# Performance work log

Measured on AMD Instinct MI355X. Metric: run time of the kernel, lower is better.

## Reference

```python
import jax, jax.numpy as jnp
import numpy as np

DIM = 2048
LAT = 512          # dim / compression_factor
NH = 16
NKV = 4
HD = LAT // NH     # 32
KVD = NKV * HD     # 128
K = 3              # conv kernel
GAIN = 0.25
EPS = 1e-6
THETA = 10000.0


def _rms(x, g):
    x32 = x.astype(jnp.float32)
    r = jax.lax.rsqrt(jnp.mean(x32 * x32, axis=-1, keepdims=True) + EPS)
    return (x32 * r).astype(x.dtype) * g.astype(x.dtype)


def _causal_conv(x, w, groups):
    # x: [B,S,C], w: [C, C//groups, K]; left-pad K-1 == pad both + trim right
    xc = jnp.transpose(x, (0, 2, 1))
    y = jax.lax.conv_general_dilated(
        xc, w, window_strides=(1,), padding=[(K - 1, 0)],
        feature_group_count=groups, dimension_numbers=('NCH', 'OIH', 'NCH'))
    return jnp.transpose(y, (0, 2, 1))


def _rope_tables(S):
    freqs = 1.0 / THETA ** (jnp.arange(0, HD, 2, dtype=jnp.float32) / HD)
    t = jnp.arange(S, dtype=jnp.float32)
    f = jnp.outer(t, freqs)               # [S, HD/2]
    return jnp.cos(f), jnp.sin(f)


def _rope(x, cos, sin):
    # x: [B,H,S,HD]; interleaved even/odd rotation
    x1, x2 = x[..., ::2], x[..., 1::2]
    r1 = x1 * cos - x2 * sin
    r2 = x1 * sin + x2 * cos
    return jnp.stack([r1, r2], axis=-1).reshape(x.shape)


def setup_inputs() -> dict:
    key = jax.random.key(0)
    ks = jax.random.split(key, 8)
    s = 0.02
    return {
        'x': jax.random.normal(ks[0], (4, 2048, DIM), jnp.float32),
        'w_q': jax.random.normal(ks[1], (LAT, DIM), jnp.float32) * s,
        'w_k': jax.random.normal(ks[2], (KVD, DIM), jnp.float32) * s,
        'w_v': jax.random.normal(ks[3], (KVD, DIM), jnp.float32) * s,
        'g_latent': jnp.ones((LAT,), jnp.float32),
        'g_kv': jnp.ones((KVD,), jnp.float32),
        'conv_q_w': jax.random.normal(ks[4], (LAT, LAT // NH, K), jnp.float32) * s,
        'conv_k_w': jax.random.normal(ks[5], (KVD, KVD // NKV, K), jnp.float32) * s,
        'g_conv': jnp.ones((LAT,), jnp.float32),
        'g_kconv': jnp.ones((KVD,), jnp.float32),
        'g_postq': jnp.ones((LAT,), jnp.float32),
        'g_postk': jnp.ones((KVD,), jnp.float32),
        'key_temp': jnp.ones((1,), jnp.float32),
        'g_preout': jnp.ones((LAT,), jnp.float32),
        'w_o': jax.random.normal(ks[6], (DIM, LAT), jnp.float32) * s,
    }


def reference(x, w_q, w_k, w_v, g_latent, g_kv, conv_q_w, conv_k_w,
              g_conv, g_kconv, g_postq, g_postk, key_temp, g_preout, w_o):
    B, S, D = x.shape
    n_groups = NH // NKV

    q = _rms(x @ w_q.T, g_latent)          # [B,S,LAT]
    k = _rms(x @ w_k.T, g_kv)              # [B,S,KVD]
    v = _rms(x @ w_v.T, g_kv)
    q_pre, k_pre = q, k

    q = _rms(_causal_conv(q, conv_q_w, NH), g_conv)
    k = _rms(_causal_conv(k, conv_k_w, NKV), g_kconv)

    # qk-mean modulation (n_groups > 1 branch)
    q_mean = q_pre.reshape(B, S, NH, HD).mean(axis=2)    # [B,S,HD]
    k_mean = k_pre.reshape(B, S, NKV, HD).mean(axis=2)   # [B,S,HD]
    q = q + GAIN * jnp.broadcast_to(k_mean[:, :, None, :], (B, S, NH, HD)).reshape(B, S, LAT)
    k = k + GAIN * jnp.broadcast_to(q_mean[:, :, None, :], (B, S, NKV, HD)).reshape(B, S, KVD)

    q = _rms(q, g_postq)
    k = _rms(k, g_postk)

    q = q.reshape(B, S, NH, HD).transpose(0, 2, 1, 3)    # [B,NH,S,HD]
    k = k.reshape(B, S, NKV, HD).transpose(0, 2, 1, 3)   # [B,NKV,S,HD]
    v = v.reshape(B, S, NKV, HD).transpose(0, 2, 1, 3)

    # QK L2 norm with learnable key temperature
    sqrt_hd = jnp.sqrt(jnp.float32(HD))
    qn = jnp.maximum(jnp.linalg.norm(q, axis=-1, keepdims=True), 1e-12)
    kn = jnp.maximum(jnp.linalg.norm(k, axis=-1, keepdims=True), 1e-12)
    q = q / qn * sqrt_hd
    k = k / kn * sqrt_hd * key_temp[0]

    cos, sin = _rope_tables(S)
    q = _rope(q, cos, sin)
    k = _rope(k, cos, sin)

    # GQA expand kv heads
    k = jnp.broadcast_to(k[:, :, None], (B, NKV, n_groups, S, HD)).reshape(B, NH, S, HD)
    v = jnp.broadcast_to(v[:, :, None], (B, NKV, n_groups, S, HD)).reshape(B, NH, S, HD)

    scale = HD ** -0.5
    scores = jnp.einsum('bhqd,bhkd->bhqk', q, k) * scale
    causal = jnp.tril(jnp.ones((S, S), bool))
    scores = jnp.where(causal, scores, jnp.finfo(scores.dtype).min)
    attn = jax.nn.softmax(scores, axis=-1)
    out = jnp.einsum('bhqk,bhkd->bhqd', attn, v)

    out = out.transpose(0, 2, 1, 3).reshape(B, S, LAT)
    out = _rms(out, g_preout)
    return out @ w_o.T
```

## Files before the change

kernel.cpp:

```cpp
#include <hip/hip_runtime.h>
#include <hip/hip_bf16.h>
#include <math.h>

constexpr int S_LEN = 2048;
constexpr int B_SZ  = 4;
constexpr int NROWS = B_SZ * S_LEN;
constexpr float GAIN_  = 0.25f;
constexpr float EPS_   = 1e-6f;
constexpr float THETA_ = 10000.0f;
constexpr float LOG2E_ = 1.44269504f;

typedef __attribute__((ext_vector_type(8))) short short8;
typedef __attribute__((ext_vector_type(4))) short sshort4;
typedef __attribute__((ext_vector_type(4))) float float4v;

__device__ __forceinline__ short f2bs(float f) {
    __hip_bfloat16 h = __float2bfloat16(f);
    short r;
    __builtin_memcpy(&r, &h, 2);
    return r;
}

__device__ __forceinline__ void async_copy16(const short* g, short* l) {
    __builtin_amdgcn_global_load_lds(
        (const __attribute__((address_space(1))) void*)g,
        (__attribute__((address_space(3))) void*)l, 16, 0, 0);
}

__device__ __forceinline__ int xcd_remap(int nwg) {
    int orig = blockIdx.x + gridDim.x * (blockIdx.y + gridDim.y * blockIdx.z);
    return (orig & 7) * (nwg >> 3) + (orig >> 3);
}

__device__ __forceinline__ float block_reduce_sum_256(float v, float* scratch) {
    __syncthreads();
    for (int off = 32; off > 0; off >>= 1)
        v += __shfl_down(v, off, 64);
    int lane = threadIdx.x & 63;
    int wid  = threadIdx.x >> 6;
    if (lane == 0) scratch[wid] = v;
    __syncthreads();
    return scratch[0] + scratch[1] + scratch[2] + scratch[3];
}

__device__ __forceinline__ void block_reduce_sum2_256(float& a, float& b, float* scratch) {
    __syncthreads();
    for (int off = 32; off > 0; off >>= 1) {
        a += __shfl_down(a, off, 64);
        b += __shfl_down(b, off, 64);
    }
    int lane = threadIdx.x & 63;
    int wid  = threadIdx.x >> 6;
    if (lane == 0) { scratch[wid] = a; scratch[4 + wid] = b; }
    __syncthreads();
    a = scratch[0] + scratch[1] + scratch[2] + scratch[3];
    b = scratch[4] + scratch[5] + scratch[6] + scratch[7];
}

__device__ __forceinline__ void block_reduce_sum3_256(float& a, float& b, float& c, float* scratch) {
    __syncthreads();
    for (int off = 32; off > 0; off >>= 1) {
        a += __shfl_down(a, off, 64);
        b += __shfl_down(b, off, 64);
        c += __shfl_down(c, off, 64);
    }
    int lane = threadIdx.x & 63;
    int wid  = threadIdx.x >> 6;
    if (lane == 0) { scratch[wid] = a; scratch[4 + wid] = b; scratch[8 + wid] = c; }
    __syncthreads();
    a = scratch[0] + scratch[1] + scratch[2] + scratch[3];
    b = scratch[4] + scratch[5] + scratch[6] + scratch[7];
    c = scratch[8] + scratch[9] + scratch[10] + scratch[11];
}

__global__ __launch_bounds__(256) void cvt_bf16(
    const float* __restrict__ src, short* __restrict__ dst, int n) {
    int i = (blockIdx.x * 256 + threadIdx.x) * 4;
    if (i >= n) return;
    float4 v = *(const float4*)(src + i);
    sshort4 o;
    o.x = f2bs(v.x); o.y = f2bs(v.y); o.z = f2bs(v.z); o.w = f2bs(v.w);
    *(sshort4*)(dst + i) = o;
}

__global__ __launch_bounds__(256) void cvt_weights(
    const float* __restrict__ wq, const float* __restrict__ wk,
    const float* __restrict__ wv, const float* __restrict__ wo,
    short* __restrict__ wqkvb, short* __restrict__ wob) {
    int i = (blockIdx.x * 256 + threadIdx.x) * 4;
    const float* src;
    short* dst;
    int j;
    if (i < 1048576)      { src = wq; dst = wqkvb + i; j = i; }
    else if (i < 1310720) { src = wk; dst = wqkvb + i; j = i - 1048576; }
    else if (i < 1572864) { src = wv; dst = wqkvb + i; j = i - 1310720; }
    else                  { src = wo; dst = wob + (i - 1572864); j = i - 1572864; }
    float4 v = *(const float4*)(src + j);
    sshort4 o;
    o.x = f2bs(v.x); o.y = f2bs(v.y); o.z = f2bs(v.z); o.w = f2bs(v.w);
    *(sshort4*)dst = o;
}

__global__ __launch_bounds__(256) void gemm_bf16_mfma(
    const short* __restrict__ A, const short* __restrict__ B,
    float* __restrict__ C, int N, int K) {
    __shared__ short As[128 * 32];
    __shared__ short Bs[128 * 32];
    int tid = threadIdx.x;
    int wave = tid >> 6, lane = tid & 63;
    int wg = xcd_remap(gridDim.x * gridDim.y);
    int bx = wg % gridDim.x, by = wg / gridDim.x;
    int m0 = by * 128, n0 = bx * 128;
    int wm = (wave >> 1) * 64, wn = (wave & 1) * 64;
    int mrow = lane & 15, quad = lane >> 4;
    float4v acc[4][4] = {};
    for (int k0 = 0; k0 < K; k0 += 32) {
        __syncthreads();
#pragma unroll
        for (int p = 0; p < 2; ++p) {
            int f = p * 256 + tid;
            int row = f >> 2, ch = (f & 3) * 8;
            const short* ga = A + (size_t)(m0 + row) * K + k0 + ch;
            const short* gb = B + (size_t)(n0 + row) * K + k0 + ch;
            async_copy16(ga, As + p * 2048 + wave * 512);
            async_copy16(gb, Bs + p * 2048 + wave * 512);
        }
        __syncthreads();
        short8 af[4], bf[4];
#pragma unroll
        for (int i = 0; i < 4; ++i)
            af[i] = *(const short8*)&As[(wm + i * 16 + mrow) * 32 + quad * 8];
#pragma unroll
        for (int j = 0; j < 4; ++j)
            bf[j] = *(const short8*)&Bs[(wn + j * 16 + mrow) * 32 + quad * 8];
#pragma unroll
        for (int i = 0; i < 4; ++i)
#pragma unroll
            for (int j = 0; j < 4; ++j)
                acc[i][j] = __builtin_amdgcn_mfma_f32_16x16x32_bf16(af[i], bf[j], acc[i][j], 0, 0, 0);
    }
#pragma unroll
    for (int i = 0; i < 4; ++i)
#pragma unroll
        for (int r = 0; r < 4; ++r) {
            int m = m0 + wm + i * 16 + quad * 4 + r;
            float* crow = C + (size_t)m * N + n0 + wn;
#pragma unroll
            for (int j = 0; j < 4; ++j)
                crow[j * 16 + mrow] = acc[i][j][r];
        }
}

__global__ __launch_bounds__(256) void gemm_bf16_mfma_sk2(
    const short* __restrict__ A, const short* __restrict__ B,
    float* __restrict__ C0, float* __restrict__ C1, int N, int K) {
    __shared__ short As[128 * 32];
    __shared__ short Bs[128 * 32];
    int tid = threadIdx.x;
    int wave = tid >> 6, lane = tid & 63;
    int wg = xcd_remap(gridDim.x * gridDim.y * gridDim.z);
    int bx = wg % gridDim.x;
    int t  = wg / gridDim.x;
    int by = t % gridDim.y;
    int bz = t / gridDim.y;
    int m0 = by * 128, n0 = bx * 128;
    int wm = (wave >> 1) * 64, wn = (wave & 1) * 64;
    int mrow = lane & 15, quad = lane >> 4;
    int kh = K >> 1;
    int kbeg = bz * kh, kend = kbeg + kh;
    float* __restrict__ C = bz ? C1 : C0;
    float4v acc[4][4] = {};
    for (int k0 = kbeg; k0 < kend; k0 += 32) {
        __syncthreads();
#pragma unroll
        for (int p = 0; p < 2; ++p) {
            int f = p * 256 + tid;
            int row = f >> 2, ch = (f & 3) * 8;
            const short* ga = A + (size_t)(m0 + row) * K + k0 + ch;
            const short* gb = B + (size_t)(n0 + row) * K + k0 + ch;
            async_copy16(ga, As + p * 2048 + wave * 512);
            async_copy16(gb, Bs + p * 2048 + wave * 512);
        }
        __syncthreads();
        short8 af[4], bf[4];
#pragma unroll
        for (int i = 0; i < 4; ++i)
            af[i] = *(const short8*)&As[(wm + i * 16 + mrow) * 32 + quad * 8];
#pragma unroll
        for (int j = 0; j < 4; ++j)
            bf[j] = *(const short8*)&Bs[(wn + j * 16 + mrow) * 32 + quad * 8];
#pragma unroll
        for (int i = 0; i < 4; ++i)
#pragma unroll
            for (int j = 0; j < 4; ++j)
                acc[i][j] = __builtin_amdgcn_mfma_f32_16x16x32_bf16(af[i], bf[j], acc[i][j], 0, 0, 0);
    }
#pragma unroll
    for (int i = 0; i < 4; ++i)
#pragma unroll
        for (int r = 0; r < 4; ++r) {
            int m = m0 + wm + i * 16 + quad * 4 + r;
            float* crow = C + (size_t)m * N + n0 + wn;
#pragma unroll
            for (int j = 0; j < 4; ++j)
                crow[j * 16 + mrow] = acc[i][j][r];
        }
}

__global__ __launch_bounds__(256) void rms_qkv_means(
    float* __restrict__ qkv, const float* __restrict__ qkv2,
    const float* __restrict__ g_latent, const float* __restrict__ g_kv,
    float* __restrict__ qmean, float* __restrict__ kmean,
    short* __restrict__ vtb) {
    int row = blockIdx.x;
    int b = row >> 11, s = row & (S_LEN - 1);
    float* p = qkv + (size_t)row * 768;
    const float* p2 = qkv2 + (size_t)row * 768;
    __shared__ float sh[640];
    __shared__ float scratch[12];
    int tid = threadIdx.x;
    float v0 = p[tid] + p2[tid];
    float v1 = p[tid + 256] + p2[tid + 256];
    float v2 = p[tid + 512] + p2[tid + 512];
    float sq = v0 * v0 + v1 * v1;
    float sk = (tid < 128) ? v2 * v2 : 0.f;
    float sv = (tid >= 128) ? v2 * v2 : 0.f;
    block_reduce_sum3_256(sq, sk, sv, scratch);
    float rq = rsqrtf(sq / 512.f + EPS_);
    float q0 = v0 * rq * g_latent[tid];
    float q1 = v1 * rq * g_latent[tid + 256];
    p[tid] = q0; p[tid + 256] = q1;
    sh[tid] = q0; sh[tid + 256] = q1;
    if (tid < 128) {
        float rk = rsqrtf(sk / 128.f + EPS_);
        float kv = v2 * rk * g_kv[tid];
        p[512 + tid] = kv; sh[512 + tid] = kv;
    } else {
        float rv = rsqrtf(sv / 128.f + EPS_);
        float vv = v2 * rv * g_kv[tid - 128];
        int d_full = tid - 128;
        vtb[((size_t)(b * 4 + (d_full >> 5)) * 32 + (d_full & 31)) * S_LEN + s] = f2bs(vv);
    }
    __syncthreads();
    if (tid < 32) {
        float sm = 0.f;
#pragma unroll
        for (int h = 0; h < 16; ++h) sm += sh[h * 32 + tid];
        qmean[(size_t)row * 32 + tid] = sm * (1.f / 16.f);
    } else if (tid < 64) {
        int d = tid - 32;
        float sm = 0.f;
#pragma unroll
        for (int h = 0; h < 4; ++h) sm += sh[512 + h * 32 + d];
        kmean[(size_t)row * 32 + d] = sm * 0.25f;
    }
}

__global__ __launch_bounds__(256) void causal_conv32(
    const float* __restrict__ in, int ldin, int inoff,
    const float* __restrict__ w, float* __restrict__ out, int C) {
    int b = blockIdx.z, g = blockIdx.y, s0 = blockIdx.x * 32;
    __shared__ float wsh[32][3][32];
    __shared__ float ish[34][33];
    int tid = threadIdx.x;
    for (int i = tid; i < 32 * 96; i += 256) {
        int oc = i / 96, r = i % 96;
        wsh[r / 3][r % 3][oc] = w[(size_t)(g * 32 + oc) * 96 + r];
    }
    for (int i = tid; i < 34 * 32; i += 256) {
        int pp = i >> 5, ic = i & 31;
        int s = s0 - 2 + pp;
        ish[pp][ic] = (s >= 0) ? in[((size_t)b * S_LEN + s) * ldin + inoff + g * 32 + ic] : 0.f;
    }
    __syncthreads();
    int sl = tid >> 3, oc0 = (tid & 7) * 4;
    float acc[4] = {0.f, 0.f, 0.f, 0.f};
    for (int ic = 0; ic < 32; ++ic) {
        float x0 = ish[sl][ic], x1 = ish[sl + 1][ic], x2 = ish[sl + 2][ic];
#pragma unroll
        for (int j = 0; j < 4; ++j)
            acc[j] += x0 * wsh[ic][0][oc0 + j] + x1 * wsh[ic][1][oc0 + j] + x2 * wsh[ic][2][oc0 + j];
    }
    float* orow = out + ((size_t)b * S_LEN + s0 + sl) * C + g * 32 + oc0;
    orow[0] = acc[0]; orow[1] = acc[1]; orow[2] = acc[2]; orow[3] = acc[3];
}

__global__ __launch_bounds__(256) void mix_rows(
    const float* __restrict__ convq, const float* __restrict__ convk,
    const float* __restrict__ qmean, const float* __restrict__ kmean,
    const float* __restrict__ g_conv, const float* __restrict__ g_kconv,
    const float* __restrict__ g_postq, const float* __restrict__ g_postk,
    const float* __restrict__ key_temp,
    short* __restrict__ qb, short* __restrict__ kb) {
    int row = blockIdx.x;
    int s = row & (S_LEN - 1);
    int tid = threadIdx.x;
    __shared__ float sh[640];
    __shared__ float scratch[8];
    __shared__ float hscale[20];
    float q0 = convq[(size_t)row * 512 + tid];
    float q1 = convq[(size_t)row * 512 + tid + 256];
    float k0 = (tid < 128) ? convk[(size_t)row * 128 + tid] : 0.f;
    float ssq = q0 * q0 + q1 * q1;
    float ssk = k0 * k0;
    block_reduce_sum2_256(ssq, ssk, scratch);
    float r1  = rsqrtf(ssq / 512.f + EPS_);
    float rk1 = rsqrtf(ssk / 128.f + EPS_);
    float km = kmean[(size_t)row * 32 + (tid & 31)];
    float a0 = q0 * r1 * g_conv[tid] + GAIN_ * km;
    float a1 = q1 * r1 * g_conv[tid + 256] + GAIN_ * km;
    float ak = 0.f;
    if (tid < 128) ak = k0 * rk1 * g_kconv[tid] + GAIN_ * qmean[(size_t)row * 32 + (tid & 31)];
    float ssq2 = a0 * a0 + a1 * a1;
    float ssk2 = ak * ak;
    block_reduce_sum2_256(ssq2, ssk2, scratch);
    float r2  = rsqrtf(ssq2 / 512.f + EPS_);
    float rk2 = rsqrtf(ssk2 / 128.f + EPS_);
    sh[tid] = a0 * r2 * g_postq[tid];
    sh[tid + 256] = a1 * r2 * g_postq[tid + 256];
    if (tid < 128) sh[512 + tid] = ak * rk2 * g_postk[tid];
    __syncthreads();
    if (tid < 16) {
        float ssh = 0.f;
        for (int d = 0; d < 32; ++d) { float x = sh[tid * 32 + d]; ssh += x * x; }
        hscale[tid] = LOG2E_ / fmaxf(sqrtf(ssh), 1e-12f);
    } else if (tid < 20) {
        int h = tid - 16;
        float ssh = 0.f;
        for (int d = 0; d < 32; ++d) { float x = sh[512 + h * 32 + d]; ssh += x * x; }
        hscale[tid] = sqrtf(32.f) / fmaxf(sqrtf(ssh), 1e-12f) * key_temp[0];
    }
    __syncthreads();
    {
        int i0 = tid * 2;
        int h = i0 >> 5;
        int fi = (i0 & 31) >> 1;
        float sc = hscale[h];
        float x1 = sh[i0] * sc, x2 = sh[i0 + 1] * sc;
        float freq = powf(THETA_, -(float)fi / 16.f);
        float ang = (float)s * freq;
        float sn, cs;
        sincosf(ang, &sn, &cs);
        unsigned lo = (unsigned short)f2bs(x1 * cs - x2 * sn);
        unsigned hi = (unsigned short)f2bs(x1 * sn + x2 * cs);
        *(unsigned*)(qb + (size_t)row * 512 + i0) = lo | (hi << 16);
    }
    if (tid < 64) {
        int i0 = tid * 2;
        int h = i0 >> 5;
        int fi = (i0 & 31) >> 1;
        float sc = hscale[16 + h];
        float x1 = sh[512 + i0] * sc, x2 = sh[512 + i0 + 1] * sc;
        float freq = powf(THETA_, -(float)fi / 16.f);
        float ang = (float)s * freq;
        float sn, cs;
        sincosf(ang, &sn, &cs);
        unsigned lo = (unsigned short)f2bs(x1 * cs - x2 * sn);
        unsigned hi = (unsigned short)f2bs(x1 * sn + x2 * cs);
        *(unsigned*)(kb + (size_t)row * 128 + i0) = lo | (hi << 16);
    }
}

__global__ __launch_bounds__(256) void attn_mfma(
    const short* __restrict__ qb, const short* __restrict__ kb,
    const short* __restrict__ vtb, float* __restrict__ OnumA,
    float* __restrict__ OnumB, float* __restrict__ LsumA,
    float* __restrict__ LsumB, const float* __restrict__ key_temp) {
    int pp = blockIdx.x, h = blockIdx.y, b = blockIdx.z;
    int pair = pp >> 1, parity = pp & 1;
    int kvh = h >> 2;
    float* __restrict__ Onum = parity ? OnumB : OnumA;
    float* __restrict__ Lsum = parity ? LsumB : LsumA;
    __shared__ short KF[2][2048];
    __shared__ short VF[2][2048];
    __shared__ __align__(16) short PF[4 * 16 * 76];
    int tid = threadIdx.x, wave = tid >> 6, lane = tid & 63;
    int cc = lane & 15, quad = lane >> 4;
    short* PFw = PF + wave * 16 * 76;
    int ldsoff = wave * 512;
    float shift2 = -5.6568543f * key_temp[0] * LOG2E_;
    float4v zinit = {shift2, shift2, shift2, shift2};
    short8 ones;
#pragma unroll
    for (int j = 0; j < 8; ++j) ones[j] = (short)0x3F80;

    const short* ksrc0 = kb +
        ((size_t)(b * S_LEN + parity * 64 + wave * 16 + (tid & 15)) * 128
         + kvh * 32 + ((tid >> 4) & 3) * 8);
    const short* vsrc0 = vtb +
        ((size_t)((b * 4 + kvh) * 32 + (wave & 1) * 16 + (tid & 15)) * S_LEN
         + parity * 64 + (tid >> 7) * 32 + ((tid >> 4) & 3) * 8);

    for (int half = 0; half < 2; ++half) {
        int qt = half ? (31 - pair) : pair;
        int s0 = qt * 64;
        short8 qfrag = *(const short8*)(qb +
            ((size_t)(b * S_LEN + s0 + wave * 16 + cc) * 512 + h * 32 + quad * 8));
        float4v accO[2];
        accO[0] = (float4v){0.f, 0.f, 0.f, 0.f};
        accO[1] = (float4v){0.f, 0.f, 0.f, 0.f};
        float4v accL = (float4v){0.f, 0.f, 0.f, 0.f};
        int qpos = s0 + wave * 16 + cc;
        const short* ksrc = ksrc0;
        const short* vsrc = vsrc0;
        int nkt = (qt - parity + 2) >> 1;

        __syncthreads();
        int cur = 0;
        if (nkt > 0) {
            async_copy16(ksrc, KF[0] + ldsoff);
            async_copy16(vsrc, VF[0] + ldsoff);
            ksrc += 2 * 64 * 128;
            vsrc += 2 * 64;
        }
        for (int it = 0; it < nkt; ++it) {
            int kt = parity + it * 2;
            __syncthreads();
            if (it + 1 < nkt) {
                async_copy16(ksrc, KF[cur ^ 1] + ldsoff);
                async_copy16(vsrc, VF[cur ^ 1] + ldsoff);
                ksrc += 2 * 64 * 128;
                vsrc += 2 * 64;
            }
            const short* KFc = KF[cur];
            const short* VFc = VF[cur];

            float4v st[4];
#pragma unroll
            for (int chunk = 0; chunk < 4; ++chunk) {
                short8 kfrag = *(const short8*)&KFc[chunk * 512 + lane * 8];
                st[chunk] = __builtin_amdgcn_mfma_f32_16x16x32_bf16(kfrag, qfrag, zinit, 0, 0, 0);
            }

            bool diag = (kt == qt);
#pragma unroll
            for (int chunk = 0; chunk < 4; ++chunk) {
                float pv[4];
#pragma unroll
                for (int r = 0; r < 4; ++r) {
                    float e = exp2f(st[chunk][r]);
                    if (diag) {
                        int kpos = kt * 64 + chunk * 16 + quad * 4 + r;
                        e = (kpos <= qpos) ? e : 0.f;
                    }
                    pv[r] = e;
                }
                unsigned u0, u1;
                asm("v_cvt_pk_bf16_f32 %0, %1, %2" : "=v"(u0) : "v"(pv[0]), "v"(pv[1]));
                asm("v_cvt_pk_bf16_f32 %0, %1, %2" : "=v"(u1) : "v"(pv[2]), "v"(pv[3]));
                *(uint2*)&PFw[cc * 76 + chunk * 16 + quad * 4] = make_uint2(u0, u1);
            }

#pragma unroll
            for (int kc = 0; kc < 2; ++kc) {
                short8 pfrag = *(const short8*)&PFw[cc * 76 + kc * 32 + quad * 8];
                accL = __builtin_amdgcn_mfma_f32_16x16x32_bf16(pfrag, ones, accL, 0, 0, 0);
#pragma unroll
                for (int dc = 0; dc < 2; ++dc) {
                    short8 vfrag = *(const short8*)&VFc[(kc * 2 + dc) * 512 + lane * 8];
                    accO[dc] = __builtin_amdgcn_mfma_f32_16x16x32_bf16(pfrag, vfrag, accO[dc], 0, 0, 0);
                }
            }
            cur ^= 1;
        }

        if (cc == 0) {
#pragma unroll
            for (int r = 0; r < 4; ++r)
                Lsum[((size_t)(b * S_LEN + s0 + wave * 16 + quad * 4 + r)) * 16 + h] = accL[r];
        }
#pragma unroll
        for (int r = 0; r < 4; ++r) {
            float* dst = Onum +
                ((size_t)(b * S_LEN + s0 + wave * 16 + quad * 4 + r) * 512 + h * 32 + cc);
            dst[0]  = accO[0][r];
            dst[16] = accO[1][r];
        }
    }
}

__global__ __launch_bounds__(256) void rms_preout_bf16(
    const float* __restrict__ OA, const float* __restrict__ OB,
    const float* __restrict__ LA, const float* __restrict__ LB,
    const float* __restrict__ g, short* __restrict__ outb) {
    int row = blockIdx.x;
    __shared__ float scratch[4];
    __shared__ float linv[16];
    int tid = threadIdx.x;
    if (tid < 16)
        linv[tid] = 1.f / (LA[(size_t)row * 16 + tid] + LB[(size_t)row * 16 + tid]);
    __syncthreads();
    float v0 = (OA[(size_t)row * 512 + tid] + OB[(size_t)row * 512 + tid]) * linv[tid >> 5];
    float v1 = (OA[(size_t)row * 512 + tid + 256] + OB[(size_t)row * 512 + tid + 256])
               * linv[(tid + 256) >> 5];
    float ssq = block_reduce_sum_256(v0 * v0 + v1 * v1, scratch);
    float r = rsqrtf(ssq / 512.f + EPS_);
    outb[(size_t)row * 512 + tid]       = f2bs(v0 * r * g[tid]);
    outb[(size_t)row * 512 + tid + 256] = f2bs(v1 * r * g[tid + 256]);
}

extern "C" void kernel_launch(void* const* d_in, const int* in_sizes, int n_in,
                              void* d_out, int out_size, void* d_ws, size_t ws_size,
                              hipStream_t stream) {
    (void)in_sizes; (void)n_in; (void)out_size; (void)ws_size;
    const float* x        = (const float*)d_in[0];
    const float* w_q      = (const float*)d_in[1];
    const float* w_k      = (const float*)d_in[2];
    const float* w_v      = (const float*)d_in[3];
    const float* g_latent = (const float*)d_in[4];
    const float* g_kv     = (const float*)d_in[5];
    const float* conv_q_w = (const float*)d_in[6];
    const float* conv_k_w = (const float*)d_in[7];
    const float* g_conv   = (const float*)d_in[8];
    const float* g_kconv  = (const float*)d_in[9];
    const float* g_postq  = (const float*)d_in[10];
    const float* g_postk  = (const float*)d_in[11];
    const float* key_temp = (const float*)d_in[12];
    const float* g_preout = (const float*)d_in[13];
    const float* w_o      = (const float*)d_in[14];
    float* out = (float*)d_out;

    char* ws = (char*)d_ws;
    const size_t R = NROWS;
    float* qkv   = (float*)ws;                        ws += R * 768 * 4;
    float* qmean = (float*)ws;                        ws += R * 32 * 4;
    float* kmean = (float*)ws;                        ws += R * 32 * 4;
    float* convq = (float*)ws;                        ws += R * 512 * 4;
    float* convk = (float*)ws;                        ws += R * 128 * 4;
    short* qbb   = (short*)ws;                        ws += R * 512 * 2;
    short* kbb   = (short*)ws;                        ws += R * 128 * 2;
    short* vtb   = (short*)ws;                        ws += R * 128 * 2;
    short* xb    = (short*)ws;                        ws += R * 2048 * 2;
    short* wqkvb = (short*)ws;                        ws += 768 * 2048 * 2;
    short* w_ob  = (short*)ws;                        ws += 2048 * 512 * 2;
    float* qkv2  = convq;
    float* OnumA = convq;
    float* OnumB = qkv;
    float* LsumA = qmean;
    float* LsumB = kmean;
    short* attnb = xb;

    dim3 blk(256);
    cvt_bf16<<<(NROWS * 2048) / 1024, blk, 0, stream>>>(x, xb, NROWS * 2048);
    cvt_weights<<<2560, blk, 0, stream>>>(w_q, w_k, w_v, w_o, wqkvb, w_ob);

    gemm_bf16_mfma_sk2<<<dim3(6, 64, 2), blk, 0, stream>>>(xb, wqkvb, qkv, qkv2, 768, 2048);
    rms_qkv_means<<<NROWS, blk, 0, stream>>>(qkv, qkv2, g_latent, g_kv, qmean, kmean, vtb);
    causal_conv32<<<dim3(64, 16, 4), blk, 0, stream>>>(qkv, 768, 0, conv_q_w, convq, 512);
    causal_conv32<<<dim3(64, 4, 4), blk, 0, stream>>>(qkv, 768, 512, conv_k_w, convk, 128);
    mix_rows<<<NROWS, blk, 0, stream>>>(convq, convk, qmean, kmean, g_conv, g_kconv,
                                        g_postq, g_postk, key_temp, qbb, kbb);
    attn_mfma<<<dim3(32, 16, 4), blk, 0, stream>>>(qbb, kbb, vtb, OnumA, OnumB,
                                                   LsumA, LsumB, key_temp);
    rms_preout_bf16<<<NROWS, blk, 0, stream>>>(OnumA, OnumB, LsumA, LsumB,
                                               g_preout, attnb);
    gemm_bf16_mfma<<<dim3(16, 64), blk, 0, stream>>>(attnb, w_ob, out, 2048, 512);
}
```

Baseline: 387.5 us.

## Drop attention KV split, normalize in-kernel to bf16, precompute RoPE table

```diff
diff --git a/kernel.cpp b/kernel.cpp
--- a/kernel.cpp
+++ b/kernel.cpp
@@ -19,6 +19,13 @@
     short r;
     __builtin_memcpy(&r, &h, 2);
     return r;
+}
+
+__device__ __forceinline__ float bs2f(short s) {
+    unsigned u = ((unsigned)(unsigned short)s) << 16;
+    float f;
+    __builtin_memcpy(&f, &u, 4);
+    return f;
 }
 
 __device__ __forceinline__ void async_copy16(const short* g, short* l) {
@@ -99,6 +106,16 @@
     sshort4 o;
     o.x = f2bs(v.x); o.y = f2bs(v.y); o.z = f2bs(v.z); o.w = f2bs(v.w);
     *(sshort4*)dst = o;
+}
+
+__global__ __launch_bounds__(256) void rope_tab(float* __restrict__ tab) {
+    int i = blockIdx.x * 256 + threadIdx.x;
+    int s = i >> 4, fi = i & 15;
+    float freq = powf(THETA_, -(float)fi / 16.f);
+    float sn, cs;
+    sincosf((float)s * freq, &sn, &cs);
+    tab[i * 2]     = cs;
+    tab[i * 2 + 1] = sn;
 }
 
 __global__ __launch_bounds__(256) void gemm_bf16_mfma(
@@ -290,7 +307,7 @@
     const float* __restrict__ qmean, const float* __restrict__ kmean,
     const float* __restrict__ g_conv, const float* __restrict__ g_kconv,
     const float* __restrict__ g_postq, const float* __restrict__ g_postk,
-    const float* __restrict__ key_temp,
+    const float* __restrict__ key_temp, const float* __restrict__ rtab,
     short* __restrict__ qb, short* __restrict__ kb) {
     int row = blockIdx.x;
     int s = row & (S_LEN - 1);
@@ -337,10 +354,8 @@
         int fi = (i0 & 31) >> 1;
         float sc = hscale[h];
         float x1 = sh[i0] * sc, x2 = sh[i0 + 1] * sc;
-        float freq = powf(THETA_, -(float)fi / 16.f);
-        float ang = (float)s * freq;
-        float sn, cs;
-        sincosf(ang, &sn, &cs);
+        float2 cssn = *(const float2*)&rtab[((size_t)s * 16 + fi) * 2];
+        float cs = cssn.x, sn = cssn.y;
         unsigned lo = (unsigned short)f2bs(x1 * cs - x2 * sn);
         unsigned hi = (unsigned short)f2bs(x1 * sn + x2 * cs);
         *(unsigned*)(qb + (size_t)row * 512 + i0) = lo | (hi << 16);
@@ -351,10 +366,8 @@
         int fi = (i0 & 31) >> 1;
         float sc = hscale[16 + h];
         float x1 = sh[512 + i0] * sc, x2 = sh[512 + i0 + 1] * sc;
-        float freq = powf(THETA_, -(float)fi / 16.f);
-        float ang = (float)s * freq;
-        float sn, cs;
-        sincosf(ang, &sn, &cs);
+        float2 cssn = *(const float2*)&rtab[((size_t)s * 16 + fi) * 2];
+        float cs = cssn.x, sn = cssn.y;
         unsigned lo = (unsigned short)f2bs(x1 * cs - x2 * sn);
         unsigned hi = (unsigned short)f2bs(x1 * sn + x2 * cs);
         *(unsigned*)(kb + (size_t)row * 128 + i0) = lo | (hi << 16);
@@ -363,20 +376,16 @@
 
 __global__ __launch_bounds__(256) void attn_mfma(
     const short* __restrict__ qb, const short* __restrict__ kb,
-    const short* __restrict__ vtb, float* __restrict__ OnumA,
-    float* __restrict__ OnumB, float* __restrict__ LsumA,
-    float* __restrict__ LsumB, const float* __restrict__ key_temp) {
-    int pp = blockIdx.x, h = blockIdx.y, b = blockIdx.z;
-    int pair = pp >> 1, parity = pp & 1;
+    const short* __restrict__ vtb, short* __restrict__ obf,
+    const float* __restrict__ key_temp) {
+    int pair = blockIdx.x, h = blockIdx.y, b = blockIdx.z;
     int kvh = h >> 2;
-    float* __restrict__ Onum = parity ? OnumB : OnumA;
-    float* __restrict__ Lsum = parity ? LsumB : LsumA;
     __shared__ short KF[2][2048];
     __shared__ short VF[2][2048];
-    __shared__ __align__(16) short PF[4 * 16 * 76];
+    __shared__ __align__(16) short PF[4 * 16 * 72];
     int tid = threadIdx.x, wave = tid >> 6, lane = tid & 63;
     int cc = lane & 15, quad = lane >> 4;
-    short* PFw = PF + wave * 16 * 76;
+    short* PFw = PF + wave * 16 * 72;
     int ldsoff = wave * 512;
     float shift2 = -5.6568543f * key_temp[0] * LOG2E_;
     float4v zinit = {shift2, shift2, shift2, shift2};
@@ -385,11 +394,11 @@
     for (int j = 0; j < 8; ++j) ones[j] = (short)0x3F80;
 
     const short* ksrc0 = kb +
-        ((size_t)(b * S_LEN + parity * 64 + wave * 16 + (tid & 15)) * 128
+        ((size_t)(b * S_LEN + wave * 16 + (tid & 15)) * 128
          + kvh * 32 + ((tid >> 4) & 3) * 8);
     const short* vsrc0 = vtb +
         ((size_t)((b * 4 + kvh) * 32 + (wave & 1) * 16 + (tid & 15)) * S_LEN
-         + parity * 64 + (tid >> 7) * 32 + ((tid >> 4) & 3) * 8);
+         + (tid >> 7) * 32 + ((tid >> 4) & 3) * 8);
 
     for (int half = 0; half < 2; ++half) {
         int qt = half ? (31 - pair) : pair;
@@ -403,24 +412,21 @@
         int qpos = s0 + wave * 16 + cc;
         const short* ksrc = ksrc0;
         const short* vsrc = vsrc0;
-        int nkt = (qt - parity + 2) >> 1;
+        int nkt = qt + 1;
 
         __syncthreads();
         int cur = 0;
-        if (nkt > 0) {
-            async_copy16(ksrc, KF[0] + ldsoff);
-            async_copy16(vsrc, VF[0] + ldsoff);
-            ksrc += 2 * 64 * 128;
-            vsrc += 2 * 64;
-        }
-        for (int it = 0; it < nkt; ++it) {
-            int kt = parity + it * 2;
+        async_copy16(ksrc, KF[0] + ldsoff);
+        async_copy16(vsrc, VF[0] + ldsoff);
+        ksrc += 64 * 128;
+        vsrc += 64;
+        for (int kt = 0; kt < nkt; ++kt) {
             __syncthreads();
-            if (it + 1 < nkt) {
+            if (kt + 1 < nkt) {
                 async_copy16(ksrc, KF[cur ^ 1] + ldsoff);
                 async_copy16(vsrc, VF[cur ^ 1] + ldsoff);
-                ksrc += 2 * 64 * 128;
-                vsrc += 2 * 64;
+                ksrc += 64 * 128;
+                vsrc += 64;
             }
             const short* KFc = KF[cur];
             const short* VFc = VF[cur];
@@ -448,12 +454,12 @@
                 unsigned u0, u1;
                 asm("v_cvt_pk_bf16_f32 %0, %1, %2" : "=v"(u0) : "v"(pv[0]), "v"(pv[1]));
                 asm("v_cvt_pk_bf16_f32 %0, %1, %2" : "=v"(u1) : "v"(pv[2]), "v"(pv[3]));
-                *(uint2*)&PFw[cc * 76 + chunk * 16 + quad * 4] = make_uint2(u0, u1);
+                *(uint2*)&PFw[cc * 72 + chunk * 16 + quad * 4] = make_uint2(u0, u1);
             }
 
 #pragma unroll
             for (int kc = 0; kc < 2; ++kc) {
-                short8 pfrag = *(const short8*)&PFw[cc * 76 + kc * 32 + quad * 8];
+                short8 pfrag = *(const short8*)&PFw[cc * 72 + kc * 32 + quad * 8];
                 accL = __builtin_amdgcn_mfma_f32_16x16x32_bf16(pfrag, ones, accL, 0, 0, 0);
 #pragma unroll
                 for (int dc = 0; dc < 2; ++dc) {
@@ -464,39 +470,31 @@
             cur ^= 1;
         }
 
-        if (cc == 0) {
-#pragma unroll
-            for (int r = 0; r < 4; ++r)
-                Lsum[((size_t)(b * S_LEN + s0 + wave * 16 + quad * 4 + r)) * 16 + h] = accL[r];
+#pragma unroll
+        for (int r = 0; r < 4; ++r) {
+            float linv = 1.f / accL[r];
+            short* dst = obf +
+                ((size_t)(b * S_LEN + s0 + wave * 16 + quad * 4 + r) * 512 + h * 32 + cc);
+            dst[0]  = f2bs(accO[0][r] * linv);
+            dst[16] = f2bs(accO[1][r] * linv);
         }
-#pragma unroll
-        for (int r = 0; r < 4; ++r) {
-            float* dst = Onum +
-                ((size_t)(b * S_LEN + s0 + wave * 16 + quad * 4 + r) * 512 + h * 32 + cc);
-            dst[0]  = accO[0][r];
-            dst[16] = accO[1][r];
-        }
     }
 }
 
 __global__ __launch_bounds__(256) void rms_preout_bf16(
-    const float* __restrict__ OA, const float* __restrict__ OB,
-    const float* __restrict__ LA, const float* __restrict__ LB,
-    const float* __restrict__ g, short* __restrict__ outb) {
+    const short* __restrict__ obf, const float* __restrict__ g,
+    short* __restrict__ outb) {
     int row = blockIdx.x;
     __shared__ float scratch[4];
-    __shared__ float linv[16];
     int tid = threadIdx.x;
-    if (tid < 16)
-        linv[tid] = 1.f / (LA[(size_t)row * 16 + tid] + LB[(size_t)row * 16 + tid]);
-    __syncthreads();
-    float v0 = (OA[(size_t)row * 512 + tid] + OB[(size_t)row * 512 + tid]) * linv[tid >> 5];
-    float v1 = (OA[(size_t)row * 512 + tid + 256] + OB[(size_t)row * 512 + tid + 256])
-               * linv[(tid + 256) >> 5];
+    unsigned pk = *(const unsigned*)(obf + (size_t)row * 512 + tid * 2);
+    float v0 = bs2f((short)(pk & 0xFFFF));
+    float v1 = bs2f((short)(pk >> 16));
     float ssq = block_reduce_sum_256(v0 * v0 + v1 * v1, scratch);
     float r = rsqrtf(ssq / 512.f + EPS_);
-    outb[(size_t)row * 512 + tid]       = f2bs(v0 * r * g[tid]);
-    outb[(size_t)row * 512 + tid + 256] = f2bs(v1 * r * g[tid + 256]);
+    unsigned lo = (unsigned short)f2bs(v0 * r * g[tid * 2]);
+    unsigned hi = (unsigned short)f2bs(v1 * r * g[tid * 2 + 1]);
+    *(unsigned*)(outb + (size_t)row * 512 + tid * 2) = lo | (hi << 16);
 }
 
 extern "C" void kernel_launch(void* const* d_in, const int* in_sizes, int n_in,
@@ -533,14 +531,13 @@
     short* xb    = (short*)ws;                        ws += R * 2048 * 2;
     short* wqkvb = (short*)ws;                        ws += 768 * 2048 * 2;
     short* w_ob  = (short*)ws;                        ws += 2048 * 512 * 2;
+    float* rtab  = (float*)ws;                        ws += 2048 * 16 * 2 * 4;
     float* qkv2  = convq;
-    float* OnumA = convq;
-    float* OnumB = qkv;
-    float* LsumA = qmean;
-    float* LsumB = kmean;
-    short* attnb = xb;
+    short* obf   = xb;
+    short* attnb = xb + R * 512;
 
     dim3 blk(256);
+    rope_tab<<<128, blk, 0, stream>>>(rtab);
     cvt_bf16<<<(NROWS * 2048) / 1024, blk, 0, stream>>>(x, xb, NROWS * 2048);
     cvt_weights<<<2560, blk, 0, stream>>>(w_q, w_k, w_v, w_o, wqkvb, w_ob);
 
@@ -549,10 +546,8 @@
     causal_conv32<<<dim3(64, 16, 4), blk, 0, stream>>>(qkv, 768, 0, conv_q_w, convq, 512);
     causal_conv32<<<dim3(64, 4, 4), blk, 0, stream>>>(qkv, 768, 512, conv_k_w, convk, 128);
     mix_rows<<<NROWS, blk, 0, stream>>>(convq, convk, qmean, kmean, g_conv, g_kconv,
-                                        g_postq, g_postk, key_temp, qbb, kbb);
-    attn_mfma<<<dim3(32, 16, 4), blk, 0, stream>>>(qbb, kbb, vtb, OnumA, OnumB,
-                                                   LsumA, LsumB, key_temp);
-    rms_preout_bf16<<<NROWS, blk, 0, stream>>>(OnumA, OnumB, LsumA, LsumB,
-                                               g_preout, attnb);
+                                        g_postq, g_postk, key_temp, rtab, qbb, kbb);
+    attn_mfma<<<dim3(16, 16, 4), blk, 0, stream>>>(qbb, kbb, vtb, obf, key_temp);
+    rms_preout_bf16<<<NROWS, blk, 0, stream>>>(obf, g_preout, attnb);
     gemm_bf16_mfma<<<dim3(16, 64), blk, 0, stream>>>(attnb, w_ob, out, 2048, 512);
 }
```

Result: faster. 365.7 us (-5.6%).
